# Kernel optimization log

Measured on AMD Instinct MI355X. Metric: run time of the kernel, lower is better.

The kernel has to match this reference:

```python
import jax, jax.numpy as jnp
import numpy as np

B, F, K, DEPTH = 512, 64, 64, 3  # feas == k == 64, deepDepth == 3


def setup_inputs() -> dict:
    key = jax.random.key(0)
    ks = jax.random.split(key, 16)
    x = jax.random.normal(ks[0], (B, F), dtype=jnp.float32)
    # wide: Linear(feas, 1)
    Ww = jax.random.normal(ks[1], (1, F), dtype=jnp.float32) * 0.1
    bw = jnp.zeros((1,), dtype=jnp.float32)
    # cross: Parameter(torch.rand(feas, k))
    cross = jax.random.uniform(ks[2], (F, K), dtype=jnp.float32)
    # attention: Linear(k, k) -> ReLU -> Linear(k, 1, bias=False)
    W1 = jax.random.normal(ks[3], (K, K), dtype=jnp.float32) / np.sqrt(K)
    b1 = jnp.zeros((K,), dtype=jnp.float32)
    w2 = jax.random.normal(ks[4], (K,), dtype=jnp.float32) / np.sqrt(K)
    # deep{i}: Linear(k//i, k//(i+1)) + ReLU, i = 1..DEPTH  -> 64->32->21->16
    dims = [K // i for i in range(1, DEPTH + 2)]  # [64, 32, 21, 16]
    Wd1 = jax.random.normal(ks[5], (dims[1], dims[0]), dtype=jnp.float32) / np.sqrt(dims[0])
    bd1 = jnp.zeros((dims[1],), dtype=jnp.float32)
    Wd2 = jax.random.normal(ks[6], (dims[2], dims[1]), dtype=jnp.float32) / np.sqrt(dims[1])
    bd2 = jnp.zeros((dims[2],), dtype=jnp.float32)
    Wd3 = jax.random.normal(ks[7], (dims[3], dims[2]), dtype=jnp.float32) / np.sqrt(dims[2])
    bd3 = jnp.zeros((dims[3],), dtype=jnp.float32)
    # out: Linear(feas // (deepDepth+1), 1) == Linear(16, 1)
    Wo = jax.random.normal(ks[8], (1, F // (DEPTH + 1)), dtype=jnp.float32) * 0.1
    bo = jnp.zeros((1,), dtype=jnp.float32)
    return {"x": x, "Ww": Ww, "bw": bw, "cross": cross, "W1": W1, "b1": b1,
            "w2": w2, "Wd1": Wd1, "bd1": bd1, "Wd2": Wd2, "bd2": bd2,
            "Wd3": Wd3, "bd3": bd3, "Wo": Wo, "bo": bo}


def reference(x, Ww, bw, cross, W1, b1, w2, Wd1, bd1, Wd2, bd2, Wd3, bd3, Wo, bo):
    linear = x @ Ww.T + bw  # [B, 1]

    # Pairwise FM interactions v[b,i,j,:] = x_i * x_j * (cross_i ∘ cross_j)
    xx = x[:, :, None] * x[:, None, :]                    # [B, F, F]
    cp = cross[:, None, :] * cross[None, :, :]            # [F, F, K]
    v = xx[..., None] * cp[None]                          # [B, F, F, K]

    # attention MLP score per pair
    h = jax.nn.relu(jnp.einsum('bijk,lk->bijl', v, W1) + b1)
    s = jnp.einsum('bijl,l->bij', h, w2)                  # [B, F, F]

    # loop semantics: upper triangle (j >= i), pair kept iff x_i != 0 and x_j != 0
    valid = jnp.triu(jnp.ones((F, F), dtype=bool))[None] \
        & (x[:, :, None] != 0) & (x[:, None, :] != 0)     # [B, F, F]
    neg = jnp.finfo(s.dtype).min
    logits = jnp.where(valid, s, neg)

    # softmax over [0 (seed zeros(1) entry), valid pair scores...];
    # the seed zeros(k) value-vector contributes nothing to the weighted sum.
    m = jnp.maximum(jnp.max(logits, axis=(1, 2)), 0.0)    # [B]
    e = jnp.where(valid, jnp.exp(logits - m[:, None, None]), 0.0)
    denom = jnp.exp(-m) + jnp.sum(e, axis=(1, 2))         # +exp(-m) is the 0-logit term
    tmp = jnp.einsum('bij,bijk->bk', e, v) / denom[:, None]  # [B, K]

    tmp = jax.nn.relu(tmp @ Wd1.T + bd1)
    tmp = jax.nn.relu(tmp @ Wd2.T + bd2)
    tmp = jax.nn.relu(tmp @ Wd3.T + bd3)
    deep_out = tmp @ Wo.T + bo                            # [B, 1]
    return jax.nn.sigmoid(linear + deep_out)
```

## Files before the change

kernel.cpp:

```cpp
#include <hip/hip_runtime.h>
#include <math.h>


#define BB 512
#define FF 64
#define NPAIRS 2080
#define THREADS 512
#define NTILES 130
#define NEG_BIG -3.402823466e38f

typedef _Float16 half8 __attribute__((ext_vector_type(8)));
typedef float f32x4 __attribute__((ext_vector_type(4)));

__global__ __launch_bounds__(THREADS, 4) void afm_r3_kernel(
    const float* __restrict__ x,
    const float* __restrict__ Ww,
    const float* __restrict__ bw,
    const float* __restrict__ cross,
    const float* __restrict__ W1,
    const float* __restrict__ b1,
    const float* __restrict__ w2,
    const float* __restrict__ Wd1,
    const float* __restrict__ bd1,
    const float* __restrict__ Wd2,
    const float* __restrict__ bd2,
    const float* __restrict__ Wd3,
    const float* __restrict__ bd3,
    const float* __restrict__ Wo,
    const float* __restrict__ bo,
    float* __restrict__ out)
{
    __shared__ __align__(16) _Float16 ah_s [FF][72];
    __shared__ __align__(16) _Float16 aht_s[FF][72];
    __shared__ __align__(16) _Float16 M_s  [FF][72];
    __shared__ float s_s[NPAIRS];
    __shared__ unsigned short lut_s[NPAIRS];
    __shared__ float x_sh[FF];
    __shared__ float part_s[4][FF];
    __shared__ float mlp_s[FF];
    __shared__ float red_s[16];
    __shared__ float scal_s[2];

    const int tid  = threadIdx.x;
    const int lane = tid & 63;
    const int wave = tid >> 6;
    const int b    = blockIdx.x;
    const int m    = lane & 15;
    const int q    = lane >> 4;

    if (tid < FF) x_sh[tid] = x[b * FF + tid];
    __syncthreads();

    for (int idx = tid; idx < FF * FF; idx += THREADS) {
        const int i = idx >> 6, k = idx & 63;
        const _Float16 v = (_Float16)(x_sh[i] * cross[idx]);
        ah_s[i][k]  = v;
        aht_s[k][i] = v;
    }
    if (tid < FF) {
        const int i = tid;
        const int basei = i * FF - (i * (i - 1)) / 2;
        const bool xi = (x_sh[i] != 0.f);
        for (int j = i; j < FF; ++j) {
            const int valid = (xi && (x_sh[j] != 0.f)) ? 0x8000 : 0;
            lut_s[basei + (j - i)] = (unsigned short)((i << 8) | j | valid);
        }
    }

    half8 afr[4][2];
    #pragma unroll
    for (int mt = 0; mt < 4; ++mt)
        #pragma unroll
        for (int kt = 0; kt < 2; ++kt) {
            const float* wr = W1 + (mt * 16 + m) * FF + kt * 32 + q * 8;
            half8 h;
            #pragma unroll
            for (int jj = 0; jj < 8; ++jj) h[jj] = (_Float16)wr[jj];
            afr[mt][kt] = h;
        }
    float b1r[16], w2r[16];
    #pragma unroll
    for (int mt = 0; mt < 4; ++mt)
        #pragma unroll
        for (int r = 0; r < 4; ++r) {
            b1r[mt * 4 + r] = b1[mt * 16 + q * 4 + r];
            w2r[mt * 4 + r] = w2[mt * 16 + q * 4 + r];
        }
    __syncthreads();

    for (int nt = wave; nt < NTILES; nt += 8) {
        const int p0 = nt * 16;
        const int ij = lut_s[p0 + m];
        const int i = (ij >> 8) & 63, j = ij & 63;
        const half8 ai0 = *(const half8*)&ah_s[i][q * 8];
        const half8 aj0 = *(const half8*)&ah_s[j][q * 8];
        const half8 ai1 = *(const half8*)&ah_s[i][32 + q * 8];
        const half8 aj1 = *(const half8*)&ah_s[j][32 + q * 8];
        const half8 bf0 = ai0 * aj0;
        const half8 bf1 = ai1 * aj1;
        float sp = 0.f;
        #pragma unroll
        for (int mt = 0; mt < 4; ++mt) {
            f32x4 acc;
            #pragma unroll
            for (int r = 0; r < 4; ++r) acc[r] = b1r[mt * 4 + r];
            acc = __builtin_amdgcn_mfma_f32_16x16x32_f16(afr[mt][0], bf0, acc, 0, 0, 0);
            acc = __builtin_amdgcn_mfma_f32_16x16x32_f16(afr[mt][1], bf1, acc, 0, 0, 0);
            #pragma unroll
            for (int r = 0; r < 4; ++r)
                sp = fmaf(w2r[mt * 4 + r], fmaxf(acc[r], 0.f), sp);
        }
        sp += __shfl_xor(sp, 16, 64);
        sp += __shfl_xor(sp, 32, 64);
        if (lane < 16) {
            const int p = p0 + lane;
            s_s[p] = (lut_s[p] & 0x8000) ? sp : NEG_BIG;
        }
    }
    __syncthreads();

    float mx = 0.0f;
    for (int p = tid; p < NPAIRS; p += THREADS) mx = fmaxf(mx, s_s[p]);
    #pragma unroll
    for (int off = 32; off > 0; off >>= 1)
        mx = fmaxf(mx, __shfl_xor(mx, off, 64));
    if (lane == 0) red_s[wave] = mx;
    __syncthreads();
    if (tid == 0) {
        float mm = red_s[0];
        for (int w = 1; w < 8; ++w) mm = fmaxf(mm, red_s[w]);
        scal_s[0] = mm;
    }
    __syncthreads();
    const float mval = scal_s[0];

    float sum = 0.f;
    for (int p = tid; p < NPAIRS; p += THREADS) {
        const float e = __expf(s_s[p] - mval);
        s_s[p] = e;
        sum += e;
    }
    #pragma unroll
    for (int off = 32; off > 0; off >>= 1)
        sum += __shfl_xor(sum, off, 64);
    if (lane == 0) red_s[8 + wave] = sum;
    __syncthreads();
    if (tid == 0) {
        float ss = __expf(-mval);
        for (int w = 0; w < 8; ++w) ss += red_s[8 + w];
        scal_s[1] = ss;
    }
    __syncthreads();
    const float denom = scal_s[1];

    for (int idx = tid; idx < FF * FF; idx += THREADS) {
        const int i = idx >> 6, j = idx & 63;
        float e = 0.f;
        if (j >= i) e = s_s[i * FF - (i * (i - 1)) / 2 + (j - i)];
        M_s[i][j] = (_Float16)e;
    }
    __syncthreads();

    {
        const int t0 = wave * 2;
        #pragma unroll
        for (int t = t0; t < t0 + 2; ++t) {
            const int i0 = (t >> 2) * 16, k0 = (t & 3) * 16;
            const half8 a0  = *(const half8*)&M_s[i0 + m][q * 8];
            const half8 a1  = *(const half8*)&M_s[i0 + m][32 + q * 8];
            const half8 bb0 = *(const half8*)&aht_s[k0 + m][q * 8];
            const half8 bb1 = *(const half8*)&aht_s[k0 + m][32 + q * 8];
            f32x4 g = {0.f, 0.f, 0.f, 0.f};
            g = __builtin_amdgcn_mfma_f32_16x16x32_f16(a0, bb0, g, 0, 0, 0);
            g = __builtin_amdgcn_mfma_f32_16x16x32_f16(a1, bb1, g, 0, 0, 0);
            const _Float16* ap = &aht_s[k0 + m][i0 + q * 4];
            float s4 = (float)ap[0] * g[0] + (float)ap[1] * g[1]
                     + (float)ap[2] * g[2] + (float)ap[3] * g[3];
            s4 += __shfl_xor(s4, 16, 64);
            s4 += __shfl_xor(s4, 32, 64);
            if (lane < 16) part_s[i0 >> 4][k0 + lane] = s4;
        }
    }
    __syncthreads();
    if (tid < FF)
        mlp_s[tid] = (part_s[0][tid] + part_s[1][tid] +
                      part_s[2][tid] + part_s[3][tid]) / denom;
    __syncthreads();

    float hv = 0.f;
    if (tid < 32) {
        float a1v = bd1[tid];
        for (int k = 0; k < 64; ++k) a1v = fmaf(Wd1[tid * 64 + k], mlp_s[k], a1v);
        hv = fmaxf(a1v, 0.f);
    }
    __syncthreads();
    if (tid < 32) mlp_s[tid] = hv;
    __syncthreads();
    if (tid < 21) {
        float a2 = bd2[tid];
        for (int k = 0; k < 32; ++k) a2 = fmaf(Wd2[tid * 32 + k], mlp_s[k], a2);
        hv = fmaxf(a2, 0.f);
    }
    __syncthreads();
    if (tid < 21) mlp_s[tid] = hv;
    __syncthreads();
    if (tid < 16) {
        float a3 = bd3[tid];
        for (int k = 0; k < 21; ++k) a3 = fmaf(Wd3[tid * 21 + k], mlp_s[k], a3);
        hv = fmaxf(a3, 0.f);
    }
    __syncthreads();
    if (tid < 16) mlp_s[tid] = hv;
    __syncthreads();

    if (tid == 0) {
        float deep = bo[0];
        for (int k = 0; k < 16; ++k) deep = fmaf(Wo[k], mlp_s[k], deep);
        float lin = bw[0];
        for (int k = 0; k < 64; ++k) lin = fmaf(Ww[k], x_sh[k], lin);
        const float z = lin + deep;
        out[b] = 1.f / (1.f + __expf(-z));
    }
}

extern "C" void kernel_launch(void* const* d_in, const int* in_sizes, int n_in,
                              void* d_out, int out_size, void* d_ws, size_t ws_size,
                              hipStream_t stream) {
    const float* xp    = (const float*)d_in[0];
    const float* Ww    = (const float*)d_in[1];
    const float* bw    = (const float*)d_in[2];
    const float* cross = (const float*)d_in[3];
    const float* W1    = (const float*)d_in[4];
    const float* b1    = (const float*)d_in[5];
    const float* w2    = (const float*)d_in[6];
    const float* Wd1   = (const float*)d_in[7];
    const float* bd1   = (const float*)d_in[8];
    const float* Wd2   = (const float*)d_in[9];
    const float* bd2   = (const float*)d_in[10];
    const float* Wd3   = (const float*)d_in[11];
    const float* bd3   = (const float*)d_in[12];
    const float* Wo    = (const float*)d_in[13];
    const float* bo    = (const float*)d_in[14];
    float* outp = (float*)d_out;

    afm_r3_kernel<<<BB, THREADS, 0, stream>>>(xp, Ww, bw, cross, W1, b1, w2,
                                              Wd1, bd1, Wd2, bd2, Wd3, bd3,
                                              Wo, bo, outp);
}
```

Baseline: 104.3 us.

## Pair two MFMA tiles per iteration and scatter softmax weights directly

The score loop now processes two 16-pair tiles per wave iteration, interleaving their MFMAs to hide latency. Max and sum reductions are finalized redundantly by every thread instead of by thread 0 plus an extra barrier. Exponentiated weights are scattered straight into a pre-zeroed M_s matrix, removing the separate triangular fill pass and two barriers. This costs more registers per thread and a zero-initialisation pass over M_s.

```diff
diff --git a/kernel.cpp b/kernel.cpp
--- a/kernel.cpp
+++ b/kernel.cpp
@@ -6,13 +6,13 @@
 #define FF 64
 #define NPAIRS 2080
 #define THREADS 512
-#define NTILES 130
+#define NIT2 65
 #define NEG_BIG -3.402823466e38f
 
 typedef _Float16 half8 __attribute__((ext_vector_type(8)));
 typedef float f32x4 __attribute__((ext_vector_type(4)));
 
-__global__ __launch_bounds__(THREADS, 4) void afm_r3_kernel(
+__global__ __launch_bounds__(THREADS, 4) void afm_r4_kernel(
     const float* __restrict__ x,
     const float* __restrict__ Ww,
     const float* __restrict__ bw,
@@ -39,7 +39,6 @@
     __shared__ float part_s[4][FF];
     __shared__ float mlp_s[FF];
     __shared__ float red_s[16];
-    __shared__ float scal_s[2];
 
     const int tid  = threadIdx.x;
     const int lane = tid & 63;
@@ -57,6 +56,8 @@
         ah_s[i][k]  = v;
         aht_s[k][i] = v;
     }
+    for (int idx = tid; idx < (FF * 72) / 2; idx += THREADS)
+        ((int*)M_s)[idx] = 0;
     if (tid < FF) {
         const int i = tid;
         const int basei = i * FF - (i * (i - 1)) / 2;
@@ -88,33 +89,39 @@
         }
     __syncthreads();
 
-    for (int nt = wave; nt < NTILES; nt += 8) {
-        const int p0 = nt * 16;
-        const int ij = lut_s[p0 + m];
-        const int i = (ij >> 8) & 63, j = ij & 63;
-        const half8 ai0 = *(const half8*)&ah_s[i][q * 8];
-        const half8 aj0 = *(const half8*)&ah_s[j][q * 8];
-        const half8 ai1 = *(const half8*)&ah_s[i][32 + q * 8];
-        const half8 aj1 = *(const half8*)&ah_s[j][32 + q * 8];
-        const half8 bf0 = ai0 * aj0;
-        const half8 bf1 = ai1 * aj1;
-        float sp = 0.f;
+    for (int it = wave; it < NIT2; it += 8) {
+        const int p0 = it * 32;
+        const int ijA = lut_s[p0 + m];
+        const int ijB = lut_s[p0 + 16 + m];
+        const int iA = (ijA >> 8) & 63, jA = ijA & 63;
+        const int iB = (ijB >> 8) & 63, jB = ijB & 63;
+        const half8 bA0 = (*(const half8*)&ah_s[iA][q * 8])      * (*(const half8*)&ah_s[jA][q * 8]);
+        const half8 bA1 = (*(const half8*)&ah_s[iA][32 + q * 8]) * (*(const half8*)&ah_s[jA][32 + q * 8]);
+        const half8 bB0 = (*(const half8*)&ah_s[iB][q * 8])      * (*(const half8*)&ah_s[jB][q * 8]);
+        const half8 bB1 = (*(const half8*)&ah_s[iB][32 + q * 8]) * (*(const half8*)&ah_s[jB][32 + q * 8]);
+        float spA = 0.f, spB = 0.f;
         #pragma unroll
         for (int mt = 0; mt < 4; ++mt) {
-            f32x4 acc;
+            f32x4 aA, aB;
             #pragma unroll
-            for (int r = 0; r < 4; ++r) acc[r] = b1r[mt * 4 + r];
-            acc = __builtin_amdgcn_mfma_f32_16x16x32_f16(afr[mt][0], bf0, acc, 0, 0, 0);
-            acc = __builtin_amdgcn_mfma_f32_16x16x32_f16(afr[mt][1], bf1, acc, 0, 0, 0);
+            for (int r = 0; r < 4; ++r) { aA[r] = b1r[mt * 4 + r]; aB[r] = b1r[mt * 4 + r]; }
+            aA = __builtin_amdgcn_mfma_f32_16x16x32_f16(afr[mt][0], bA0, aA, 0, 0, 0);
+            aB = __builtin_amdgcn_mfma_f32_16x16x32_f16(afr[mt][0], bB0, aB, 0, 0, 0);
+            aA = __builtin_amdgcn_mfma_f32_16x16x32_f16(afr[mt][1], bA1, aA, 0, 0, 0);
+            aB = __builtin_amdgcn_mfma_f32_16x16x32_f16(afr[mt][1], bB1, aB, 0, 0, 0);
             #pragma unroll
-            for (int r = 0; r < 4; ++r)
-                sp = fmaf(w2r[mt * 4 + r], fmaxf(acc[r], 0.f), sp);
-        }
-        sp += __shfl_xor(sp, 16, 64);
-        sp += __shfl_xor(sp, 32, 64);
+            for (int r = 0; r < 4; ++r) {
+                spA = fmaf(w2r[mt * 4 + r], fmaxf(aA[r], 0.f), spA);
+                spB = fmaf(w2r[mt * 4 + r], fmaxf(aB[r], 0.f), spB);
+            }
+        }
+        spA += __shfl_xor(spA, 16, 64);
+        spA += __shfl_xor(spA, 32, 64);
+        spB += __shfl_xor(spB, 16, 64);
+        spB += __shfl_xor(spB, 32, 64);
         if (lane < 16) {
-            const int p = p0 + lane;
-            s_s[p] = (lut_s[p] & 0x8000) ? sp : NEG_BIG;
+            s_s[p0 + lane]      = (ijA & 0x8000) ? spA : NEG_BIG;
+            s_s[p0 + 16 + lane] = (ijB & 0x8000) ? spB : NEG_BIG;
         }
     }
     __syncthreads();
@@ -126,40 +133,25 @@
         mx = fmaxf(mx, __shfl_xor(mx, off, 64));
     if (lane == 0) red_s[wave] = mx;
     __syncthreads();
-    if (tid == 0) {
-        float mm = red_s[0];
-        for (int w = 1; w < 8; ++w) mm = fmaxf(mm, red_s[w]);
-        scal_s[0] = mm;
-    }
-    __syncthreads();
-    const float mval = scal_s[0];
+    float mval = red_s[0];
+    #pragma unroll
+    for (int w = 1; w < 8; ++w) mval = fmaxf(mval, red_s[w]);
 
     float sum = 0.f;
     for (int p = tid; p < NPAIRS; p += THREADS) {
+        const int ij = lut_s[p];
         const float e = __expf(s_s[p] - mval);
-        s_s[p] = e;
         sum += e;
+        M_s[(ij >> 8) & 63][ij & 63] = (_Float16)e;
     }
     #pragma unroll
     for (int off = 32; off > 0; off >>= 1)
         sum += __shfl_xor(sum, off, 64);
     if (lane == 0) red_s[8 + wave] = sum;
     __syncthreads();
-    if (tid == 0) {
-        float ss = __expf(-mval);
-        for (int w = 0; w < 8; ++w) ss += red_s[8 + w];
-        scal_s[1] = ss;
-    }
-    __syncthreads();
-    const float denom = scal_s[1];
-
-    for (int idx = tid; idx < FF * FF; idx += THREADS) {
-        const int i = idx >> 6, j = idx & 63;
-        float e = 0.f;
-        if (j >= i) e = s_s[i * FF - (i * (i - 1)) / 2 + (j - i)];
-        M_s[i][j] = (_Float16)e;
-    }
-    __syncthreads();
+    float denom = __expf(-mval);
+    #pragma unroll
+    for (int w = 0; w < 8; ++w) denom += red_s[8 + w];
 
     {
         const int t0 = wave * 2;
@@ -243,7 +235,7 @@
     const float* bo    = (const float*)d_in[14];
     float* outp = (float*)d_out;
 
-    afm_r3_kernel<<<BB, THREADS, 0, stream>>>(xp, Ww, bw, cross, W1, b1, w2,
+    afm_r4_kernel<<<BB, THREADS, 0, stream>>>(xp, Ww, bw, cross, W1, b1, w2,
                                               Wd1, bd1, Wd2, bd2, Wd3, bd3,
                                               Wo, bo, outp);
 }
```

After: 103.4 us. No clear change (-0.9%).
